# Optimization experiments

Hardware: AMD Instinct MI355X
Metric: run time of the kernel (lower is better)

The kernel has to match this reference:

```python
import jax, jax.numpy as jnp
import numpy as np

B, S, H, NH = 1, 2048, 768, 12
HD = H // NH  # 64


def setup_inputs() -> dict:
    key = jax.random.key(0)
    k0, k1, k2, k3 = jax.random.split(key, 4)
    BN = B * S
    return {
        "hidden_states": jax.random.normal(k0, (B, S, H), dtype=jnp.float32),
        "g": jax.random.uniform(k1, (BN, BN), dtype=jnp.float32),
        "attention_mask": jnp.zeros((B, S), dtype=jnp.float32),
        "Wq": jax.random.normal(k2, (H, H), dtype=jnp.float32) * 0.02,
        "bq": jnp.zeros((H,), dtype=jnp.float32),
        "Wv": jax.random.normal(k3, (H, H), dtype=jnp.float32) * 0.02,
        "bv": jnp.zeros((H,), dtype=jnp.float32),
    }


def reference(hidden_states, g, attention_mask, Wq, bq, Wv, bv):
    # hidden_states: [B, S, H] -> torch code transposes to [S, B, H]
    hs = jnp.swapaxes(hidden_states, 0, 1)  # [S, B, H]
    s, b, h = hs.shape
    BN = s * b

    q = hs @ Wq.T + bq  # [S, B, H]
    v = hs @ Wv.T + bv  # [S, B, H]

    # view(S,B,NH,HD).transpose(0,1) -> [B,S,NH,HD], then flat reshape to [NH, BN, HD]
    q = jnp.swapaxes(q.reshape(s, b, NH, HD), 0, 1).reshape(NH, BN, HD)
    # L2-normalize each query vector along head_dim (torch F.normalize, eps=1e-12)
    q = q / jnp.maximum(jnp.linalg.norm(q, axis=2, keepdims=True), 1e-12)

    # value: [B,S,NH,HD] flattened to [BN, NH, HD]
    v = jnp.swapaxes(v.reshape(s, b, NH, HD), 0, 1).reshape(BN, NH, HD)

    # attn sparsification mask combine (computed in original, but never used downstream)
    bool_mask = (attention_mask >= 0).reshape(-1, 1).astype(g.dtype)  # [BN, 1]
    _g_masked = g * (bool_mask @ bool_mask.T)  # dead value, kept for faithfulness

    # L2-distance attention scores: -(AA - 2AB + BB) / sqrt(head_dim)
    AB = jnp.einsum('hnd,hmd->hnm', q, q)            # [NH, BN, BN]
    AA = jnp.sum(q * q, axis=-1, keepdims=True)      # [NH, BN, 1]
    sim = -(AA - 2.0 * AB + jnp.swapaxes(AA, -1, -2)) * (HD ** -0.5)
    attn = jax.nn.softmax(sim, axis=-1)              # [NH, BN, BN]

    # weighted value sum: bmm(attn, v.transpose(0,1)) -> [NH, BN, HD]
    out = jnp.einsum('hnm,hmd->hnd', attn, jnp.swapaxes(v, 0, 1))

    # reshape(B,S,NH,HD) then merge last two dims -> [B, S, H]
    out = out.reshape(b, s, NH, HD).reshape(b, s, h)
    return out
```

## Files before the change

### kernel.cpp

```cpp
#include <hip/hip_runtime.h>
#include <math.h>

#define NTOK 2048
#define HDIM 768
#define NHEAD 12
#define NQ (NTOK * NHEAD)

typedef __attribute__((ext_vector_type(8))) short short8v;
typedef __attribute__((ext_vector_type(4))) float float4v;

static __device__ __forceinline__ unsigned short f2bf(float x) {
    unsigned u = __float_as_uint(x);
    return (unsigned short)((u + 0x7fffu + ((u >> 16) & 1u)) >> 16);
}
static __device__ __forceinline__ unsigned pk2(float a, float b) {
    unsigned r;
    asm("v_cvt_pk_bf16_f32 %0, %1, %2" : "=v"(r) : "v"(a), "v"(b));
    return r;
}
static __device__ __forceinline__ void gload_lds16(const void* g, void* lds_uniform) {
    __builtin_amdgcn_global_load_lds(
        (const __attribute__((address_space(1))) void*)g,
        (__attribute__((address_space(3))) void*)lds_uniform, 16, 0, 0);
}

__global__ __launch_bounds__(256) void projnorm_kernel(
    const float* __restrict__ hs, const float* __restrict__ Wq,
    const float* __restrict__ bq, const float* __restrict__ Wv,
    const float* __restrict__ bv, unsigned short* __restrict__ qbf,
    unsigned short* __restrict__ vT)
{
    constexpr int PITCH = 40;
    __shared__ unsigned short As[2][128 * PITCH];
    __shared__ unsigned short Bs[2][64 * PITCH];

    const bool isq = (blockIdx.z == 0);
    const float* W    = isq ? Wq : Wv;
    const float* bias = isq ? bq : bv;
    const int n0 = blockIdx.x * 64, m0 = blockIdx.y * 128;
    const int tid = threadIdx.x, lane = tid & 63, w = tid >> 6;

    const int arow = tid >> 1, acol = (tid & 1) * 16;
    const int brow = tid >> 2, bcol = (tid & 3) * 8;
    const float* ag = hs + (size_t)(m0 + arow) * HDIM + acol;
    const float* bg = W + (size_t)(n0 + brow) * HDIM + bcol;

    float4 ga[4], gb[2];
#define PLOAD(k0)                                                              \
    {                                                                          \
        _Pragma("unroll") for (int i = 0; i < 4; ++i)                          \
            ga[i] = *(const float4*)(ag + (k0) + i * 4);                       \
        _Pragma("unroll") for (int i = 0; i < 2; ++i)                          \
            gb[i] = *(const float4*)(bg + (k0) + i * 4);                       \
    }
#define PCVTW(b)                                                               \
    {                                                                          \
        uint4 u0 = {pk2(ga[0].x, ga[0].y), pk2(ga[0].z, ga[0].w),              \
                    pk2(ga[1].x, ga[1].y), pk2(ga[1].z, ga[1].w)};             \
        uint4 u1 = {pk2(ga[2].x, ga[2].y), pk2(ga[2].z, ga[2].w),              \
                    pk2(ga[3].x, ga[3].y), pk2(ga[3].z, ga[3].w)};             \
        *(uint4*)&As[b][arow * PITCH + acol]     = u0;                         \
        *(uint4*)&As[b][arow * PITCH + acol + 8] = u1;                         \
        uint4 u2 = {pk2(gb[0].x, gb[0].y), pk2(gb[0].z, gb[0].w),              \
                    pk2(gb[1].x, gb[1].y), pk2(gb[1].z, gb[1].w)};             \
        *(uint4*)&Bs[b][brow * PITCH + bcol] = u2;                             \
    }

    float4v acc[2][4];
    #pragma unroll
    for (int fr = 0; fr < 2; ++fr)
        #pragma unroll
        for (int fc = 0; fc < 4; ++fc) acc[fr][fc] = (float4v){0.f, 0.f, 0.f, 0.f};

    PLOAD(0);
    PCVTW(0);

    for (int ks = 0; ks < 24; ++ks) {
        const int b = ks & 1;
        if (ks < 23) PLOAD((ks + 1) * 32);
        __syncthreads();
        short8v af[2], bf[4];
        #pragma unroll
        for (int fr = 0; fr < 2; ++fr)
            af[fr] = *(const short8v*)
                &As[b][(w * 32 + fr * 16 + (lane & 15)) * PITCH + ((lane >> 4) << 3)];
        #pragma unroll
        for (int fc = 0; fc < 4; ++fc)
            bf[fc] = *(const short8v*)
                &Bs[b][(fc * 16 + (lane & 15)) * PITCH + ((lane >> 4) << 3)];
        #pragma unroll
        for (int fr = 0; fr < 2; ++fr)
            #pragma unroll
            for (int fc = 0; fc < 4; ++fc)
                acc[fr][fc] = __builtin_amdgcn_mfma_f32_16x16x32_bf16(
                    af[fr], bf[fc], acc[fr][fc], 0, 0, 0);
        if (ks < 23) PCVTW(b ^ 1);
    }
#undef PLOAD
#undef PCVTW

    float bcol4[4];
    #pragma unroll
    for (int fc = 0; fc < 4; ++fc) bcol4[fc] = bias[n0 + fc * 16 + (lane & 15)];

    if (isq) {
        #pragma unroll
        for (int fr = 0; fr < 2; ++fr)
            #pragma unroll
            for (int r = 0; r < 4; ++r) {
                float v[4];
                float ss = 0.f;
                #pragma unroll
                for (int fc = 0; fc < 4; ++fc) {
                    v[fc] = acc[fr][fc][r] + bcol4[fc];
                    ss = fmaf(v[fc], v[fc], ss);
                }
                ss += __shfl_xor(ss, 1);
                ss += __shfl_xor(ss, 2);
                ss += __shfl_xor(ss, 4);
                ss += __shfl_xor(ss, 8);
                float inv = 1.0f / fmaxf(sqrtf(ss), 1e-12f);
                int m = m0 + w * 32 + fr * 16 + ((lane >> 4) << 2) + r;
                #pragma unroll
                for (int fc = 0; fc < 4; ++fc)
                    qbf[(size_t)m * HDIM + n0 + fc * 16 + (lane & 15)] = f2bf(v[fc] * inv);
            }
    } else {
        #pragma unroll
        for (int fr = 0; fr < 2; ++fr)
            #pragma unroll
            for (int fc = 0; fc < 4; ++fc) {
                int f = n0 + fc * 16 + (lane & 15);
                int mtk = m0 + w * 32 + fr * 16 + ((lane >> 4) << 2);
                union { unsigned short u[4]; unsigned long long q; } pk;
                #pragma unroll
                for (int r = 0; r < 4; ++r) pk.u[r] = f2bf(acc[fr][fc][r] + bcol4[fc]);
                *(unsigned long long*)(vT + (size_t)f * NTOK + mtk) = pk.q;
            }
    }
}

__global__ __launch_bounds__(128, 3) void attn_kernel(
    const unsigned short* __restrict__ qbf,
    const unsigned short* __restrict__ vT,
    float* __restrict__ num0,
    float* __restrict__ part1,
    float* __restrict__ lbuf)
{
    __shared__ unsigned short Ksb[2][64 * 64];
    __shared__ unsigned short Pl[2][16 * 72];

    const int bid = blockIdx.x;
    const int swz = (bid & 7) * 192 + (bid >> 3);
    const int h = swz >> 7, rem = swz & 127;
    const int qt = rem >> 1, ksp = rem & 1;
    const int tid = threadIdx.x, lane = tid & 63, w = tid >> 6;
    const int n0 = qt * 32;
    const int kbase0 = ksp * 1024;

    const unsigned short* kh = qbf + (size_t)h * NTOK * 64;
    const unsigned short* vh = vT + (size_t)h * 64 * NTOK;

    const unsigned short* qrow = kh + ((size_t)n0 + w * 16 + (lane & 15)) * 64;
    short8v qa[2];
    qa[0] = *(const short8v*)(qrow + ((lane >> 4) << 3));
    qa[1] = *(const short8v*)(qrow + 32 + ((lane >> 4) << 3));

#define STAGE_K(buf, m0v)                                                      \
    {                                                                          \
        _Pragma("unroll")                                                      \
        for (int i = 0; i < 4; ++i) {           \
            int ci = ((w * 4 + i) << 6) + lane;                                \
            int r = ci >> 3, c8 = (ci & 7) ^ (r & 7);                          \
            gload_lds16(kh + ((size_t)(m0v) + r) * 64 + (c8 << 3),             \
                        (char*)&Ksb[buf][0] + ((w * 4 + i) << 10));            \
        }                                                                      \
    }
    short8v vf[8];
#define LOADV(mb)                                                              \
    _Pragma("unroll")                                                          \
    for (int t = 0; t < 4; ++t)                                                \
        _Pragma("unroll")                                                      \
        for (int kk = 0; kk < 2; ++kk)                                         \
            vf[t * 2 + kk] = *(const short8v*)(                                \
                vh + (size_t)(t * 16 + (lane & 15)) * NTOK + (mb) +            \
                kk * 32 + ((lane >> 4) << 3));

    float4v acc[4];
    #pragma unroll
    for (int t = 0; t < 4; ++t) acc[t] = (float4v){0.f, 0.f, 0.f, 0.f};
    float lsum = 0.f;

    STAGE_K(0, kbase0);
    LOADV(kbase0);
    __syncthreads();

    for (int mt = 0; mt < 16; ++mt) {
        const int cur = mt & 1;
        if (mt < 15) STAGE_K(cur ^ 1, kbase0 + (mt + 1) * 64);

        float4v St[4];
        __builtin_amdgcn_s_setprio(1);
        #pragma unroll
        for (int t = 0; t < 4; ++t) {
            St[t] = (float4v){0.f, 0.f, 0.f, 0.f};
            #pragma unroll
            for (int kk = 0; kk < 2; ++kk) {
                int row = (lane & 15) + (t << 4);
                int off = ((row << 7) + (kk << 6) + ((lane >> 4) << 4)) ^ ((row & 7) << 4);
                short8v kf = *(const short8v*)((const char*)&Ksb[cur][0] + off);
                St[t] = __builtin_amdgcn_mfma_f32_16x16x32_bf16(kf, qa[kk], St[t], 0, 0, 0);
            }
        }
        __builtin_amdgcn_s_setprio(0);

        float p[4][4];
        float ls = 0.f;
        #pragma unroll
        for (int t = 0; t < 4; ++t)
            #pragma unroll
            for (int r = 0; r < 4; ++r) {
                p[t][r] = __expf(St[t][r] * 0.25f);
                ls += p[t][r];
            }
        ls += __shfl_xor(ls, 16);
        ls += __shfl_xor(ls, 32);
        lsum += ls;

        #pragma unroll
        for (int t = 0; t < 4; ++t) {
            unsigned w0 = pk2(p[t][0], p[t][1]);
            unsigned w1 = pk2(p[t][2], p[t][3]);
            unsigned long long q64 =
                (unsigned long long)w0 | ((unsigned long long)w1 << 32);
            *(unsigned long long*)(&Pl[w][(lane & 15) * 72 + t * 16 +
                                          ((lane >> 4) << 2)]) = q64;
        }
        asm volatile("s_waitcnt lgkmcnt(0)" ::: "memory");
        __builtin_amdgcn_sched_barrier(0);
        short8v pf[2];
        #pragma unroll
        for (int kk = 0; kk < 2; ++kk)
            pf[kk] = *(const short8v*)(&Pl[w][(lane & 15) * 72 + kk * 32 +
                                              ((lane >> 4) << 3)]);

        __builtin_amdgcn_s_setprio(1);
        #pragma unroll
        for (int t = 0; t < 4; ++t) {
            acc[t] = __builtin_amdgcn_mfma_f32_16x16x32_bf16(pf[0], vf[t*2+0], acc[t], 0, 0, 0);
            acc[t] = __builtin_amdgcn_mfma_f32_16x16x32_bf16(pf[1], vf[t*2+1], acc[t], 0, 0, 0);
        }
        __builtin_amdgcn_s_setprio(0);

        if (mt < 15) {
            LOADV(kbase0 + (mt + 1) * 64);
            asm volatile("s_waitcnt vmcnt(8)" ::: "memory");
            __builtin_amdgcn_s_barrier();
            __builtin_amdgcn_sched_barrier(0);
        }
    }
#undef STAGE_K
#undef LOADV

    float* nout = ksp ? part1 : num0;
    #pragma unroll
    for (int r = 0; r < 4; ++r) {
        int n = n0 + w * 16 + ((lane >> 4) << 2) + r;
        #pragma unroll
        for (int t = 0; t < 4; ++t)
            nout[((size_t)h * NTOK + n) * 64 + t * 16 + (lane & 15)] = acc[t][r];
    }
    if (lane < 16)
        lbuf[ksp * NQ + h * NTOK + n0 + w * 16 + lane] = lsum;
}

__global__ __launch_bounds__(256) void combine_kernel(
    float* __restrict__ out, const float* __restrict__ part1,
    const float* __restrict__ lbuf)
{
    int gid = blockIdx.x * 256 + threadIdx.x;
    float4 a = ((const float4*)out)[gid];
    float4 b = ((const float4*)part1)[gid];
    int row = gid >> 4;
    float inv = 1.0f / (lbuf[row] + lbuf[NQ + row]);
    float4 o;
    o.x = (a.x + b.x) * inv; o.y = (a.y + b.y) * inv;
    o.z = (a.z + b.z) * inv; o.w = (a.w + b.w) * inv;
    ((float4*)out)[gid] = o;
}

extern "C" void kernel_launch(void* const* d_in, const int* in_sizes, int n_in,
                              void* d_out, int out_size, void* d_ws, size_t ws_size,
                              hipStream_t stream)
{
    const float* hs = (const float*)d_in[0];
    const float* Wq = (const float*)d_in[3];
    const float* bq = (const float*)d_in[4];
    const float* Wv = (const float*)d_in[5];
    const float* bv = (const float*)d_in[6];
    float* out = (float*)d_out;

    unsigned short* qbf   = (unsigned short*)d_ws;
    unsigned short* vT    = qbf + (size_t)NTOK * HDIM;
    float*          part1 = (float*)(vT + (size_t)HDIM * NTOK);
    float*          lbuf  = part1 + (size_t)NQ * 64;

    projnorm_kernel<<<dim3(12, 16, 2), 256, 0, stream>>>(
        hs, Wq, bq, Wv, bv, qbf, vT);
    attn_kernel<<<dim3(1536), 128, 0, stream>>>(qbf, vT, out, part1, lbuf);
    combine_kernel<<<dim3(1536), 256, 0, stream>>>(out, part1, lbuf);
}
```

Baseline: 154.5 us.

## Double-buffer V fragments in registers and issue next-tile loads up front

Splits the V fragment registers into two ping-pong sets and unrolls the attention loop by two. The next tile's K staging and V loads are now issued at the start of each tile instead of after the PV MFMAs, so global-load latency overlaps the whole QK, softmax and PV sequence. The launch hint changes from min-blocks 3 to amdgpu_waves_per_eu(3,3), which constrains register allocation differently. The extra 32 VGPRs for the second V buffer add register pressure and could cause spills under that occupancy target.

```diff
diff --git a/kernel.cpp b/kernel.cpp
--- a/kernel.cpp
+++ b/kernel.cpp
@@ -140,7 +140,9 @@
     }
 }
 
-__global__ __launch_bounds__(128, 3) void attn_kernel(
+__global__ __launch_bounds__(128)
+__attribute__((amdgpu_waves_per_eu(3, 3)))
+void attn_kernel(
     const unsigned short* __restrict__ qbf,
     const unsigned short* __restrict__ vT,
     float* __restrict__ num0,
@@ -176,13 +178,13 @@
                         (char*)&Ksb[buf][0] + ((w * 4 + i) << 10));            \
         }                                                                      \
     }
-    short8v vf[8];
-#define LOADV(mb)                                                              \
+    short8v vfA[8], vfB[8];
+#define LOADV(VF, mb)                                                          \
     _Pragma("unroll")                                                          \
     for (int t = 0; t < 4; ++t)                                                \
         _Pragma("unroll")                                                      \
         for (int kk = 0; kk < 2; ++kk)                                         \
-            vf[t * 2 + kk] = *(const short8v*)(                                \
+            VF[t * 2 + kk] = *(const short8v*)(                                \
                 vh + (size_t)(t * 16 + (lane & 15)) * NTOK + (mb) +            \
                 kk * 32 + ((lane >> 4) << 3));
 
@@ -191,74 +193,90 @@
     for (int t = 0; t < 4; ++t) acc[t] = (float4v){0.f, 0.f, 0.f, 0.f};
     float lsum = 0.f;
 
+#define TILE_BODY(MT, KB, VFC, VFN, LAST)                                      \
+    {                                                                          \
+        if (!(LAST)) {                                                         \
+            STAGE_K((KB) ^ 1, kbase0 + ((MT) + 1) * 64);                       \
+            LOADV(VFN, kbase0 + ((MT) + 1) * 64);                              \
+            __builtin_amdgcn_sched_barrier(0);            \
+        }                                                                      \
+                     \
+        float4v St[4];                                                         \
+        __builtin_amdgcn_s_setprio(1);                                         \
+        _Pragma("unroll")                                                      \
+        for (int t = 0; t < 4; ++t) {                                          \
+            St[t] = (float4v){0.f, 0.f, 0.f, 0.f};                             \
+            _Pragma("unroll")                                                  \
+            for (int kk = 0; kk < 2; ++kk) {                                   \
+                int row = (lane & 15) + (t << 4);                              \
+                int off = ((row << 7) + (kk << 6) + ((lane >> 4) << 4)) ^      \
+                          ((row & 7) << 4);                                    \
+                short8v kf = *(const short8v*)((const char*)&Ksb[KB][0] + off);\
+                St[t] = __builtin_amdgcn_mfma_f32_16x16x32_bf16(               \
+                    kf, qa[kk], St[t], 0, 0, 0);                               \
+            }                                                                  \
+        }                                                                      \
+        __builtin_amdgcn_s_setprio(0);                                         \
+                     \
+        float p[4][4];                                                         \
+        float ls = 0.f;                                                        \
+        _Pragma("unroll")                                                      \
+        for (int t = 0; t < 4; ++t)                                            \
+            _Pragma("unroll")                                                  \
+            for (int r = 0; r < 4; ++r) {                                      \
+                p[t][r] = __expf(St[t][r] * 0.25f);                            \
+                ls += p[t][r];                                                 \
+            }                                                                  \
+        ls += __shfl_xor(ls, 16);                                              \
+        ls += __shfl_xor(ls, 32);                                              \
+        lsum += ls;                                                            \
+                         \
+        _Pragma("unroll")                                                      \
+        for (int t = 0; t < 4; ++t) {                                          \
+            unsigned w0 = pk2(p[t][0], p[t][1]);                               \
+            unsigned w1 = pk2(p[t][2], p[t][3]);                               \
+            unsigned long long q64 =                                           \
+                (unsigned long long)w0 | ((unsigned long long)w1 << 32);       \
+            *(unsigned long long*)(&Pl[w][(lane & 15) * 72 + t * 16 +          \
+                                          ((lane >> 4) << 2)]) = q64;          \
+        }                                                                      \
+        asm volatile("s_waitcnt lgkmcnt(0)" ::: "memory");                     \
+        __builtin_amdgcn_sched_barrier(0);                                     \
+        short8v pf[2];                                                         \
+        _Pragma("unroll")                                                      \
+        for (int kk = 0; kk < 2; ++kk)                                         \
+            pf[kk] = *(const short8v*)(&Pl[w][(lane & 15) * 72 + kk * 32 +     \
+                                              ((lane >> 4) << 3)]);            \
+         \
+        __builtin_amdgcn_s_setprio(1);                                         \
+        _Pragma("unroll")                                                      \
+        for (int t = 0; t < 4; ++t) {                                          \
+            acc[t] = __builtin_amdgcn_mfma_f32_16x16x32_bf16(                  \
+                pf[0], VFC[t * 2 + 0], acc[t], 0, 0, 0);                       \
+            acc[t] = __builtin_amdgcn_mfma_f32_16x16x32_bf16(                  \
+                pf[1], VFC[t * 2 + 1], acc[t], 0, 0, 0);                       \
+        }                                                                      \
+        __builtin_amdgcn_s_setprio(0);                                         \
+        if (!(LAST)) {                                                         \
+            asm volatile("s_waitcnt vmcnt(8)" ::: "memory");   \
+            __builtin_amdgcn_s_barrier();                  \
+            __builtin_amdgcn_sched_barrier(0);                                 \
+        }                                                                      \
+    }
+
     STAGE_K(0, kbase0);
-    LOADV(kbase0);
+    LOADV(vfA, kbase0);
     __syncthreads();
 
-    for (int mt = 0; mt < 16; ++mt) {
-        const int cur = mt & 1;
-        if (mt < 15) STAGE_K(cur ^ 1, kbase0 + (mt + 1) * 64);
-
-        float4v St[4];
-        __builtin_amdgcn_s_setprio(1);
-        #pragma unroll
-        for (int t = 0; t < 4; ++t) {
-            St[t] = (float4v){0.f, 0.f, 0.f, 0.f};
-            #pragma unroll
-            for (int kk = 0; kk < 2; ++kk) {
-                int row = (lane & 15) + (t << 4);
-                int off = ((row << 7) + (kk << 6) + ((lane >> 4) << 4)) ^ ((row & 7) << 4);
-                short8v kf = *(const short8v*)((const char*)&Ksb[cur][0] + off);
-                St[t] = __builtin_amdgcn_mfma_f32_16x16x32_bf16(kf, qa[kk], St[t], 0, 0, 0);
-            }
+    for (int it = 0; it < 8; ++it) {
+        TILE_BODY(2 * it,     0, vfA, vfB, false);
+        if (it < 7) {
+            TILE_BODY(2 * it + 1, 1, vfB, vfA, false);
+        } else {
+            TILE_BODY(2 * it + 1, 1, vfB, vfA, true);
         }
-        __builtin_amdgcn_s_setprio(0);
-
-        float p[4][4];
-        float ls = 0.f;
-        #pragma unroll
-        for (int t = 0; t < 4; ++t)
-            #pragma unroll
-            for (int r = 0; r < 4; ++r) {
-                p[t][r] = __expf(St[t][r] * 0.25f);
-                ls += p[t][r];
-            }
-        ls += __shfl_xor(ls, 16);
-        ls += __shfl_xor(ls, 32);
-        lsum += ls;
-
-        #pragma unroll
-        for (int t = 0; t < 4; ++t) {
-            unsigned w0 = pk2(p[t][0], p[t][1]);
-            unsigned w1 = pk2(p[t][2], p[t][3]);
-            unsigned long long q64 =
-                (unsigned long long)w0 | ((unsigned long long)w1 << 32);
-            *(unsigned long long*)(&Pl[w][(lane & 15) * 72 + t * 16 +
-                                          ((lane >> 4) << 2)]) = q64;
-        }
-        asm volatile("s_waitcnt lgkmcnt(0)" ::: "memory");
-        __builtin_amdgcn_sched_barrier(0);
-        short8v pf[2];
-        #pragma unroll
-        for (int kk = 0; kk < 2; ++kk)
-            pf[kk] = *(const short8v*)(&Pl[w][(lane & 15) * 72 + kk * 32 +
-                                              ((lane >> 4) << 3)]);
-
-        __builtin_amdgcn_s_setprio(1);
-        #pragma unroll
-        for (int t = 0; t < 4; ++t) {
-            acc[t] = __builtin_amdgcn_mfma_f32_16x16x32_bf16(pf[0], vf[t*2+0], acc[t], 0, 0, 0);
-            acc[t] = __builtin_amdgcn_mfma_f32_16x16x32_bf16(pf[1], vf[t*2+1], acc[t], 0, 0, 0);
-        }
-        __builtin_amdgcn_s_setprio(0);
-
-        if (mt < 15) {
-            LOADV(kbase0 + (mt + 1) * 64);
-            asm volatile("s_waitcnt vmcnt(8)" ::: "memory");
-            __builtin_amdgcn_s_barrier();
-            __builtin_amdgcn_sched_barrier(0);
-        }
-    }
+    }
+#undef TILE_BODY
 #undef STAGE_K
 #undef LOADV
 
```

New measurement: 153.9 us. Within noise of the previous version (-0.3%).

## Load K fragments directly from global memory, dropping LDS staging and prefetch

Applied to the files above, without the earlier changes.

The attention kernel no longer stages K tiles into double-buffered shared memory with global_load_lds. Each wave now loads its K and V fragments straight from global into registers at the top of every iteration, which removes the block barriers, the LDS traffic and the software prefetch. In exchange, each wave issues duplicate global loads for K with no overlap across iterations and has to rely on occupancy and cache hits to hide latency. The occupancy hint changes to amdgpu_waves_per_eu(3,3).

```diff
diff --git a/kernel.cpp b/kernel.cpp
--- a/kernel.cpp
+++ b/kernel.cpp
@@ -17,11 +17,6 @@
     unsigned r;
     asm("v_cvt_pk_bf16_f32 %0, %1, %2" : "=v"(r) : "v"(a), "v"(b));
     return r;
-}
-static __device__ __forceinline__ void gload_lds16(const void* g, void* lds_uniform) {
-    __builtin_amdgcn_global_load_lds(
-        (const __attribute__((address_space(1))) void*)g,
-        (__attribute__((address_space(3))) void*)lds_uniform, 16, 0, 0);
 }
 
 __global__ __launch_bounds__(256) void projnorm_kernel(
@@ -140,14 +135,15 @@
     }
 }
 
-__global__ __launch_bounds__(128, 3) void attn_kernel(
+__global__ __launch_bounds__(128)
+__attribute__((amdgpu_waves_per_eu(3, 3)))
+void attn_kernel(
     const unsigned short* __restrict__ qbf,
     const unsigned short* __restrict__ vT,
     float* __restrict__ num0,
     float* __restrict__ part1,
     float* __restrict__ lbuf)
 {
-    __shared__ unsigned short Ksb[2][64 * 64];
     __shared__ unsigned short Pl[2][16 * 72];
 
     const int bid = blockIdx.x;
@@ -166,51 +162,39 @@
     qa[0] = *(const short8v*)(qrow + ((lane >> 4) << 3));
     qa[1] = *(const short8v*)(qrow + 32 + ((lane >> 4) << 3));
 
-#define STAGE_K(buf, m0v)                                                      \
-    {                                                                          \
-        _Pragma("unroll")                                                      \
-        for (int i = 0; i < 4; ++i) {           \
-            int ci = ((w * 4 + i) << 6) + lane;                                \
-            int r = ci >> 3, c8 = (ci & 7) ^ (r & 7);                          \
-            gload_lds16(kh + ((size_t)(m0v) + r) * 64 + (c8 << 3),             \
-                        (char*)&Ksb[buf][0] + ((w * 4 + i) << 10));            \
-        }                                                                      \
-    }
-    short8v vf[8];
-#define LOADV(mb)                                                              \
-    _Pragma("unroll")                                                          \
-    for (int t = 0; t < 4; ++t)                                                \
-        _Pragma("unroll")                                                      \
-        for (int kk = 0; kk < 2; ++kk)                                         \
-            vf[t * 2 + kk] = *(const short8v*)(                                \
-                vh + (size_t)(t * 16 + (lane & 15)) * NTOK + (mb) +            \
-                kk * 32 + ((lane >> 4) << 3));
-
     float4v acc[4];
     #pragma unroll
     for (int t = 0; t < 4; ++t) acc[t] = (float4v){0.f, 0.f, 0.f, 0.f};
     float lsum = 0.f;
 
-    STAGE_K(0, kbase0);
-    LOADV(kbase0);
-    __syncthreads();
-
     for (int mt = 0; mt < 16; ++mt) {
-        const int cur = mt & 1;
-        if (mt < 15) STAGE_K(cur ^ 1, kbase0 + (mt + 1) * 64);
+        const int mb = kbase0 + mt * 64;
+
+        short8v kf[8], vf[8];
+        #pragma unroll
+        for (int t = 0; t < 4; ++t)
+            #pragma unroll
+            for (int kk = 0; kk < 2; ++kk)
+                kf[t * 2 + kk] = *(const short8v*)(
+                    kh + ((size_t)(mb + t * 16 + (lane & 15))) * 64 +
+                    kk * 32 + ((lane >> 4) << 3));
+        #pragma unroll
+        for (int t = 0; t < 4; ++t)
+            #pragma unroll
+            for (int kk = 0; kk < 2; ++kk)
+                vf[t * 2 + kk] = *(const short8v*)(
+                    vh + (size_t)(t * 16 + (lane & 15)) * NTOK + mb +
+                    kk * 32 + ((lane >> 4) << 3));
 
         float4v St[4];
         __builtin_amdgcn_s_setprio(1);
         #pragma unroll
         for (int t = 0; t < 4; ++t) {
             St[t] = (float4v){0.f, 0.f, 0.f, 0.f};
-            #pragma unroll
-            for (int kk = 0; kk < 2; ++kk) {
-                int row = (lane & 15) + (t << 4);
-                int off = ((row << 7) + (kk << 6) + ((lane >> 4) << 4)) ^ ((row & 7) << 4);
-                short8v kf = *(const short8v*)((const char*)&Ksb[cur][0] + off);
-                St[t] = __builtin_amdgcn_mfma_f32_16x16x32_bf16(kf, qa[kk], St[t], 0, 0, 0);
-            }
+            St[t] = __builtin_amdgcn_mfma_f32_16x16x32_bf16(
+                kf[t * 2 + 0], qa[0], St[t], 0, 0, 0);
+            St[t] = __builtin_amdgcn_mfma_f32_16x16x32_bf16(
+                kf[t * 2 + 1], qa[1], St[t], 0, 0, 0);
         }
         __builtin_amdgcn_s_setprio(0);
 
@@ -236,8 +220,6 @@
             *(unsigned long long*)(&Pl[w][(lane & 15) * 72 + t * 16 +
                                           ((lane >> 4) << 2)]) = q64;
         }
-        asm volatile("s_waitcnt lgkmcnt(0)" ::: "memory");
-        __builtin_amdgcn_sched_barrier(0);
         short8v pf[2];
         #pragma unroll
         for (int kk = 0; kk < 2; ++kk)
@@ -247,20 +229,13 @@
         __builtin_amdgcn_s_setprio(1);
         #pragma unroll
         for (int t = 0; t < 4; ++t) {
-            acc[t] = __builtin_amdgcn_mfma_f32_16x16x32_bf16(pf[0], vf[t*2+0], acc[t], 0, 0, 0);
-            acc[t] = __builtin_amdgcn_mfma_f32_16x16x32_bf16(pf[1], vf[t*2+1], acc[t], 0, 0, 0);
+            acc[t] = __builtin_amdgcn_mfma_f32_16x16x32_bf16(
+                pf[0], vf[t * 2 + 0], acc[t], 0, 0, 0);
+            acc[t] = __builtin_amdgcn_mfma_f32_16x16x32_bf16(
+                pf[1], vf[t * 2 + 1], acc[t], 0, 0, 0);
         }
         __builtin_amdgcn_s_setprio(0);
-
-        if (mt < 15) {
-            LOADV(kbase0 + (mt + 1) * 64);
-            asm volatile("s_waitcnt vmcnt(8)" ::: "memory");
-            __builtin_amdgcn_s_barrier();
-            __builtin_amdgcn_sched_barrier(0);
-        }
-    }
-#undef STAGE_K
-#undef LOADV
+    }
 
     float* nout = ksp ? part1 : num0;
     #pragma unroll
```

Result: slower. 187.9 us (+21.7%).
